# Kernel tuning notes

Hardware: AMD Instinct MI355X
Metric: run time of the kernel (lower is better)

The kernel has to match this reference:

```python
import jax, jax.numpy as jnp
import numpy as np

B, TK, N = 32, 2048, 1024  # batch, encoder steps, 2*hidden_dim


def setup_inputs() -> dict:
    key = jax.random.key(0)
    ks = jax.random.split(key, 12)
    s = 0.02
    return {
        "s_t_hat": jax.random.normal(ks[0], (B, N), jnp.float32),
        "h": jax.random.normal(ks[1], (B, TK, N), jnp.float32),
        "enc_padding_mask": jax.random.uniform(ks[2], (B, TK), jnp.float32),
        "coverage": jax.random.uniform(ks[3], (B, TK), jnp.float32),
        "q_h": jax.random.normal(ks[4], (B, TK, N), jnp.float32),
        "W_h": jax.random.normal(ks[5], (N, N), jnp.float32) * s,
        "W_q": jax.random.normal(ks[6], (N, N), jnp.float32) * s,
        "W_c": jax.random.normal(ks[7], (N,), jnp.float32) * s,   # Linear(1, N) weight, squeezed
        "W_d": jax.random.normal(ks[8], (N, N), jnp.float32) * s,  # decode_proj weight
        "b_d": jnp.zeros((N,), jnp.float32),                       # decode_proj bias
        "v_w": jax.random.normal(ks[9], (N,), jnp.float32) * s,    # v: Linear(N, 1) weight, squeezed
    }


def reference(s_t_hat, h, enc_padding_mask, coverage, q_h, W_h, W_q, W_c, W_d, b_d, v_w):
    # projections (Linear: y = x @ W.T)
    enc_feat = jnp.einsum("btn,mn->btm", h, W_h)            # [B,TK,N]
    q_feat = jnp.einsum("btn,mn->btm", q_h, W_q)            # [B,TK,N]
    dec_feat = s_t_hat @ W_d.T + b_d                         # [B,N]
    cov_feat = coverage[..., None] * W_c                     # [B,TK,N]
    att = jnp.tanh(enc_feat + dec_feat[:, None, :] + q_feat + cov_feat)
    scores = jnp.einsum("btn,n->bt", att, v_w)               # [B,TK]
    attn_ = jax.nn.softmax(scores, axis=1) * enc_padding_mask
    attn = attn_ / jnp.sum(attn_, axis=1, keepdims=True)     # renormalized
    c_t = jnp.einsum("bt,btn->bn", attn, h)                  # context vector
    coverage_out = coverage + attn
    return (c_t, attn, coverage_out)
```

## Files before the change

### kernel.cpp

```cpp
#include <hip/hip_runtime.h>
#include <stdint.h>

#define Bsz 32
#define TKs 2048
#define Nf  1024
#define Msz (Bsz*TKs)
#define KTOT 2048

typedef __bf16 bf16x8 __attribute__((ext_vector_type(8)));
typedef float  f32x4  __attribute__((ext_vector_type(4)));

__device__ __forceinline__ unsigned pack_bf2(float f0, float f1){
  unsigned u0 = __float_as_uint(f0) + 0x8000u;
  unsigned u1 = __float_as_uint(f1) + 0x8000u;
  return __builtin_amdgcn_perm(u1, u0, 0x07060302u);
}

__device__ __forceinline__ float fast_tanh(float x){
  x = fminf(15.f, fmaxf(-15.f, x));
  float e = __expf(2.f * x);
  return (e - 1.f) / (e + 1.f);
}

__device__ __forceinline__ void async16(void* lds, const void* g){
  __builtin_amdgcn_global_load_lds(
      (const __attribute__((address_space(1))) unsigned int*)g,
      (__attribute__((address_space(3))) unsigned int*)lds,
      16, 0, 0);
}

__global__ __launch_bounds__(256) void pack_w_kernel(
    const float* __restrict__ Wh, const float* __restrict__ Wq,
    unsigned short* __restrict__ Wcat)
{
  int idx = (blockIdx.x * 256 + threadIdx.x) * 4;
  int m = idx >> 11;
  int k = idx & 2047;
  const float* src = (k < 1024) ? (Wh + m * 1024 + k) : (Wq + m * 1024 + (k - 1024));
  float4 v = *(const float4*)src;
  uint2 p;
  p.x = pack_bf2(v.x, v.y);
  p.y = pack_bf2(v.z, v.w);
  *(uint2*)(Wcat + idx) = p;
}

__global__ __launch_bounds__(256) void pack_a_kernel(
    const float* __restrict__ h, const float* __restrict__ q,
    unsigned short* __restrict__ Acat)
{
  size_t idx = ((size_t)blockIdx.x * 256 + threadIdx.x) * 8;
  size_t r = idx >> 11;
  int c = (int)(idx & 2047);
  const float* src = (c < 1024) ? (h + r * 1024 + c) : (q + r * 1024 + (c - 1024));
  float4 v0 = ((const float4*)src)[0];
  float4 v1 = ((const float4*)src)[1];
  uint4 p;
  p.x = pack_bf2(v0.x, v0.y); p.y = pack_bf2(v0.z, v0.w);
  p.z = pack_bf2(v1.x, v1.y); p.w = pack_bf2(v1.z, v1.w);
  *(uint4*)(Acat + idx) = p;
}

__global__ __launch_bounds__(256) void dec_kernel(
    const float* __restrict__ s_t, const float* __restrict__ Wd,
    const float* __restrict__ bd, float* __restrict__ dec)
{
  __shared__ float sv[1024];
  const int b = blockIdx.y;
  const int mbase = blockIdx.x * 64;
  for (int i = threadIdx.x; i < 1024; i += 256) sv[i] = s_t[b * 1024 + i];
  __syncthreads();
  const int wave = threadIdx.x >> 6, lane = threadIdx.x & 63;
  #pragma unroll 4
  for (int i = 0; i < 16; ++i){
    int m = mbase + wave * 16 + i;
    const float4* wr = (const float4*)(Wd + (size_t)m * 1024 + lane * 16);
    const float4* sr = (const float4*)(sv + lane * 16);
    float s = 0.f;
    #pragma unroll
    for (int j = 0; j < 4; ++j){
      float4 w = wr[j], x = sr[j];
      s += w.x * x.x + w.y * x.y + w.z * x.z + w.w * x.w;
    }
    #pragma unroll
    for (int d = 1; d < 64; d <<= 1) s += __shfl_xor(s, d);
    if (lane == 0) dec[b * 1024 + m] = s + bd[m];
  }
}

__global__ __launch_bounds__(256) void gemm_fused_fast(
    const unsigned short* __restrict__ Acat,
    const unsigned short* __restrict__ Wcat,
    const float* __restrict__ dec, const float* __restrict__ cov,
    const float* __restrict__ Wc, const float* __restrict__ vw,
    float* __restrict__ scoresP)
{
  __shared__ __align__(16) unsigned short As[128 * 32];
  __shared__ __align__(16) unsigned short Bs[128 * 32];
  __shared__ float ssum[2][128];

  const int tid  = threadIdx.x;
  const int wave = tid >> 6, lane = tid & 63;
  const int wm = wave & 1, wn = wave >> 1;
  const int quad = lane >> 4, low = lane & 15;

  const int p = blockIdx.x;
  const int ntile = (p >> 3) & 7;
  const int mtile = (p & 7) + ((p >> 6) << 3);

  f32x4 acc[4][4];
  #pragma unroll
  for (int i = 0; i < 4; ++i)
    #pragma unroll
    for (int j = 0; j < 4; ++j) acc[i][j] = (f32x4){0.f, 0.f, 0.f, 0.f};

  const int s0 = wave * 128 + lane;
  const int s1 = s0 + 64;
  const unsigned short* pA0 = Acat + (size_t)(mtile * 128 + (s0 >> 2)) * 2048 + (s0 & 3) * 8;
  const unsigned short* pA1 = Acat + (size_t)(mtile * 128 + (s1 >> 2)) * 2048 + (s1 & 3) * 8;
  const unsigned short* pB0 = Wcat + (size_t)(ntile * 128 + (s0 >> 2)) * 2048 + (s0 & 3) * 8;
  const unsigned short* pB1 = Wcat + (size_t)(ntile * 128 + (s1 >> 2)) * 2048 + (s1 & 3) * 8;
  unsigned short* ldsA0 = &As[wave * 512];
  unsigned short* ldsA1 = &As[wave * 512 + 256];
  ldsA1 = &As[wave * 1024 + 512];
  ldsA0 = &As[wave * 1024];
  unsigned short* ldsB0 = &Bs[wave * 1024];
  unsigned short* ldsB1 = &Bs[wave * 1024 + 512];

  const bf16x8* a_rd[4];
  const bf16x8* b_rd[4];
  #pragma unroll
  for (int i = 0; i < 4; ++i){
    a_rd[i] = (const bf16x8*)&As[(wm * 64 + i * 16 + low) * 32 + quad * 8];
    b_rd[i] = (const bf16x8*)&Bs[(wn * 64 + i * 16 + low) * 32 + quad * 8];
  }

  for (int kt = 0; kt < KTOT / 32; ++kt){
    async16(ldsA0, pA0);
    async16(ldsA1, pA1);
    async16(ldsB0, pB0);
    async16(ldsB1, pB1);
    pA0 += 32; pA1 += 32; pB0 += 32; pB1 += 32;
    __syncthreads();
    bf16x8 af[4], bg[4];
    #pragma unroll
    for (int i = 0; i < 4; ++i){ af[i] = *a_rd[i]; bg[i] = *b_rd[i]; }
    #pragma unroll
    for (int mi = 0; mi < 4; ++mi)
      #pragma unroll
      for (int ni = 0; ni < 4; ++ni)
        acc[mi][ni] = __builtin_amdgcn_mfma_f32_16x16x32_bf16(af[mi], bg[ni], acc[mi][ni], 0, 0, 0);
    __syncthreads();
  }

  const int brow = (mtile * 128) >> 11;
  const float* decb = dec + brow * 1024;
  const int colbase = ntile * 128 + wn * 64 + low;
  float dv[4], wc4[4], vw4[4];
  #pragma unroll
  for (int ni = 0; ni < 4; ++ni){
    int col = colbase + ni * 16;
    dv[ni]  = decb[col];
    wc4[ni] = Wc[col];
    vw4[ni] = vw[col];
  }
  const size_t growbase = (size_t)mtile * 128;
  const int rowloc0 = wm * 64 + quad * 4;
  #pragma unroll
  for (int mi = 0; mi < 4; ++mi){
    #pragma unroll
    for (int r = 0; r < 4; ++r){
      int rl = rowloc0 + mi * 16 + r;
      float cv = cov[growbase + rl];
      float s = 0.f;
      #pragma unroll
      for (int ni = 0; ni < 4; ++ni){
        float x = acc[mi][ni][r] + dv[ni] + cv * wc4[ni];
        s += vw4[ni] * fast_tanh(x);
      }
      #pragma unroll
      for (int d = 1; d < 16; d <<= 1) s += __shfl_xor(s, d);
      if (low == 0) ssum[wn][rl] = s;
    }
  }
  __syncthreads();
  if (tid < 128)
    scoresP[(size_t)ntile * Msz + growbase + tid] = ssum[0][tid] + ssum[1][tid];
}

#define AST 40

__global__ __launch_bounds__(256) void gemm_fused_fb(
    const float* __restrict__ h, const float* __restrict__ q,
    const unsigned short* __restrict__ Wcat,
    const float* __restrict__ dec, const float* __restrict__ cov,
    const float* __restrict__ Wc, const float* __restrict__ vw,
    float* __restrict__ scoresP)
{
  __shared__ unsigned short As[128 * AST];
  __shared__ unsigned short Bs[128 * AST];
  __shared__ float ssum[2][128];

  const int tid  = threadIdx.x;
  const int wave = tid >> 6, lane = tid & 63;
  const int wm = wave & 1, wn = wave >> 1;
  const int quad = lane >> 4, low = lane & 15;
  const int ntile = blockIdx.x;
  const int mtile = blockIdx.y;

  f32x4 acc[4][4];
  #pragma unroll
  for (int i = 0; i < 4; ++i)
    #pragma unroll
    for (int j = 0; j < 4; ++j) acc[i][j] = (f32x4){0.f, 0.f, 0.f, 0.f};

  const int sr = tid >> 1;
  const int sh = (tid & 1) * 16;
  const size_t a_goff = ((size_t)(mtile * 128 + sr)) * 1024 + sh;
  const size_t b_goff = ((size_t)(ntile * 128 + sr)) * 2048 + sh;
  unsigned short* a_st = &As[sr * AST + sh];
  unsigned short* b_st = &Bs[sr * AST + sh];

  const bf16x8* a_rd[4];
  const bf16x8* b_rd[4];
  #pragma unroll
  for (int i = 0; i < 4; ++i){
    a_rd[i] = (const bf16x8*)&As[(wm * 64 + i * 16 + low) * AST + quad * 8];
    b_rd[i] = (const bf16x8*)&Bs[(wn * 64 + i * 16 + low) * AST + quad * 8];
  }

  for (int kt = 0; kt < KTOT / 32; ++kt){
    const int k0 = kt * 32;
    {
      const float* src = (k0 < 1024) ? (h + a_goff + k0) : (q + a_goff + (k0 - 1024));
      float4 v0 = ((const float4*)src)[0];
      float4 v1 = ((const float4*)src)[1];
      float4 v2 = ((const float4*)src)[2];
      float4 v3 = ((const float4*)src)[3];
      uint4 p0, p1;
      p0.x = pack_bf2(v0.x, v0.y); p0.y = pack_bf2(v0.z, v0.w);
      p0.z = pack_bf2(v1.x, v1.y); p0.w = pack_bf2(v1.z, v1.w);
      p1.x = pack_bf2(v2.x, v2.y); p1.y = pack_bf2(v2.z, v2.w);
      p1.z = pack_bf2(v3.x, v3.y); p1.w = pack_bf2(v3.z, v3.w);
      ((uint4*)a_st)[0] = p0;
      ((uint4*)a_st)[1] = p1;
    }
    {
      const uint4* src = (const uint4*)(Wcat + b_goff + k0);
      uint4 w0 = src[0];
      uint4 w1 = src[1];
      ((uint4*)b_st)[0] = w0;
      ((uint4*)b_st)[1] = w1;
    }
    __syncthreads();
    bf16x8 af[4], bg[4];
    #pragma unroll
    for (int i = 0; i < 4; ++i){ af[i] = *a_rd[i]; bg[i] = *b_rd[i]; }
    #pragma unroll
    for (int mi = 0; mi < 4; ++mi)
      #pragma unroll
      for (int ni = 0; ni < 4; ++ni)
        acc[mi][ni] = __builtin_amdgcn_mfma_f32_16x16x32_bf16(af[mi], bg[ni], acc[mi][ni], 0, 0, 0);
    __syncthreads();
  }

  const int brow = (mtile * 128) >> 11;
  const float* decb = dec + brow * 1024;
  const int colbase = ntile * 128 + wn * 64 + low;
  float dv[4], wc4[4], vw4[4];
  #pragma unroll
  for (int ni = 0; ni < 4; ++ni){
    int col = colbase + ni * 16;
    dv[ni]  = decb[col];
    wc4[ni] = Wc[col];
    vw4[ni] = vw[col];
  }
  const size_t growbase = (size_t)mtile * 128;
  const int rowloc0 = wm * 64 + quad * 4;
  #pragma unroll
  for (int mi = 0; mi < 4; ++mi){
    #pragma unroll
    for (int r = 0; r < 4; ++r){
      int rl = rowloc0 + mi * 16 + r;
      float cv = cov[growbase + rl];
      float s = 0.f;
      #pragma unroll
      for (int ni = 0; ni < 4; ++ni){
        float x = acc[mi][ni][r] + dv[ni] + cv * wc4[ni];
        s += vw4[ni] * fast_tanh(x);
      }
      #pragma unroll
      for (int d = 1; d < 16; d <<= 1) s += __shfl_xor(s, d);
      if (low == 0) ssum[wn][rl] = s;
    }
  }
  __syncthreads();
  if (tid < 128)
    scoresP[(size_t)ntile * Msz + growbase + tid] = ssum[0][tid] + ssum[1][tid];
}

__global__ __launch_bounds__(256) void softmax_kernel(
    const float* __restrict__ scoresP, const float* __restrict__ mask,
    const float* __restrict__ cov, float* __restrict__ attn_o,
    float* __restrict__ cov_o)
{
  const int b = blockIdx.x;
  const int tid = threadIdx.x;
  const int wave = tid >> 6, lane = tid & 63;
  __shared__ float redm[4], reds[4];
  float sc[8];
  float mx = -3.4e38f;
  #pragma unroll
  for (int j = 0; j < 8; ++j){
    int t = tid + j * 256;
    float s = 0.f;
    #pragma unroll
    for (int p = 0; p < 8; ++p) s += scoresP[(size_t)p * Msz + b * TKs + t];
    sc[j] = s;
    mx = fmaxf(mx, s);
  }
  #pragma unroll
  for (int d = 1; d < 64; d <<= 1) mx = fmaxf(mx, __shfl_xor(mx, d));
  if (lane == 0) redm[wave] = mx;
  __syncthreads();
  mx = fmaxf(fmaxf(redm[0], redm[1]), fmaxf(redm[2], redm[3]));
  float e[8]; float sum = 0.f;
  #pragma unroll
  for (int j = 0; j < 8; ++j){
    int t = tid + j * 256;
    float v = __expf(sc[j] - mx) * mask[b * TKs + t];
    e[j] = v; sum += v;
  }
  #pragma unroll
  for (int d = 1; d < 64; d <<= 1) sum += __shfl_xor(sum, d);
  if (lane == 0) reds[wave] = sum;
  __syncthreads();
  sum = reds[0] + reds[1] + reds[2] + reds[3];
  float inv = 1.f / sum;
  #pragma unroll
  for (int j = 0; j < 8; ++j){
    int t = tid + j * 256;
    float a = e[j] * inv;
    attn_o[b * TKs + t] = a;
    cov_o[b * TKs + t]  = cov[b * TKs + t] + a;
  }
}

__global__ __launch_bounds__(256) void ct_partial(
    const float* __restrict__ h, const float* __restrict__ attn,
    float* __restrict__ P)
{
  const int b = blockIdx.y, tc = blockIdx.x;
  const int n4 = threadIdx.x * 4;
  float4 acc = {0.f, 0.f, 0.f, 0.f};
  const float* hb = h + ((size_t)b * TKs + tc * 64) * Nf;
  const float* ab = attn + b * TKs + tc * 64;
  #pragma unroll 4
  for (int tt = 0; tt < 64; ++tt){
    float a = ab[tt];
    float4 hv = *(const float4*)(hb + (size_t)tt * Nf + n4);
    acc.x += a * hv.x; acc.y += a * hv.y; acc.z += a * hv.z; acc.w += a * hv.w;
  }
  *(float4*)(P + ((size_t)(tc * Bsz + b)) * Nf + n4) = acc;
}

__global__ __launch_bounds__(256) void ct_reduce(
    const float* __restrict__ P, float* __restrict__ out)
{
  int bn = (blockIdx.x * 256 + threadIdx.x) * 4;
  float4 s = {0.f, 0.f, 0.f, 0.f};
  for (int j = 0; j < 32; ++j){
    float4 v = *(const float4*)(P + (size_t)j * (Bsz * Nf) + bn);
    s.x += v.x; s.y += v.y; s.z += v.z; s.w += v.w;
  }
  *(float4*)(out + bn) = s;
}

extern "C" void kernel_launch(void* const* d_in, const int* in_sizes, int n_in,
                              void* d_out, int out_size, void* d_ws, size_t ws_size,
                              hipStream_t stream) {
  const float* s_t  = (const float*)d_in[0];
  const float* h    = (const float*)d_in[1];
  const float* mask = (const float*)d_in[2];
  const float* cov  = (const float*)d_in[3];
  const float* qh   = (const float*)d_in[4];
  const float* Wh   = (const float*)d_in[5];
  const float* Wq   = (const float*)d_in[6];
  const float* Wc   = (const float*)d_in[7];
  const float* Wd   = (const float*)d_in[8];
  const float* bd   = (const float*)d_in[9];
  const float* vw   = (const float*)d_in[10];

  float* out    = (float*)d_out;
  float* c_t    = out;
  float* attn_o = out + Bsz * Nf;
  float* cov_o  = attn_o + Bsz * TKs;

  char* ws = (char*)d_ws;
  unsigned short* Wcat = (unsigned short*)ws;
  float* dec     = (float*)(ws + (4u << 20));
  float* scoresP = (float*)(ws + (4u << 20) + (128u << 10));
  float* ctP     = (float*)(ws + (6u << 20) + (128u << 10));
  unsigned short* Acat = (unsigned short*)(ws + (16ull << 20));

  const size_t need_fast = (16ull << 20) + (size_t)Msz * KTOT * 2;
  const bool fast = (ws_size >= need_fast);

  hipLaunchKernelGGL(pack_w_kernel, dim3(2048), dim3(256), 0, stream, Wh, Wq, Wcat);
  hipLaunchKernelGGL(dec_kernel,    dim3(16, 32), dim3(256), 0, stream, s_t, Wd, bd, dec);
  if (fast){
    hipLaunchKernelGGL(pack_a_kernel, dim3((unsigned)((size_t)Msz * KTOT / 8 / 256)),
                       dim3(256), 0, stream, h, qh, Acat);
    hipLaunchKernelGGL(gemm_fused_fast, dim3(4096), dim3(256), 0, stream,
                       Acat, Wcat, dec, cov, Wc, vw, scoresP);
  } else {
    hipLaunchKernelGGL(gemm_fused_fb, dim3(8, 512), dim3(256), 0, stream,
                       h, qh, Wcat, dec, cov, Wc, vw, scoresP);
  }
  hipLaunchKernelGGL(softmax_kernel, dim3(32), dim3(256), 0, stream,
                     scoresP, mask, cov, attn_o, cov_o);
  hipLaunchKernelGGL(ct_partial, dim3(32, 32), dim3(256), 0, stream, h, attn_o, ctP);
  hipLaunchKernelGGL(ct_reduce,  dim3(32), dim3(256), 0, stream, ctP, c_t);
}
```

Baseline: 992.0 us.

## Switch GEMM to 32x32 MFMA with swizzled LDS, read bf16 h for context

The fused score GEMM moves from 16x16x32 to 32x32x16 bf16 MFMA tiles, and the LDS layout gets an XOR swizzle to reduce bank conflicts. Coverage is staged in shared memory, and tanh uses a reciprocal intrinsic with no clamp. The context-vector partial kernel now reads the bf16 packed copy of h (Acat) instead of fp32 h, roughly halving its traffic. In exchange c_t is computed from bf16-rounded h, which lowers its precision, and the unclamped tanh could give inf/NaN for large inputs in edge cases.

```diff
diff --git a/kernel.cpp b/kernel.cpp
--- a/kernel.cpp
+++ b/kernel.cpp
@@ -9,6 +9,7 @@
 
 typedef __bf16 bf16x8 __attribute__((ext_vector_type(8)));
 typedef float  f32x4  __attribute__((ext_vector_type(4)));
+typedef float  f32x16 __attribute__((ext_vector_type(16)));
 
 __device__ __forceinline__ unsigned pack_bf2(float f0, float f1){
   unsigned u0 = __float_as_uint(f0) + 0x8000u;
@@ -17,9 +18,8 @@
 }
 
 __device__ __forceinline__ float fast_tanh(float x){
-  x = fminf(15.f, fmaxf(-15.f, x));
   float e = __expf(2.f * x);
-  return (e - 1.f) / (e + 1.f);
+  return 1.f - 2.f * __builtin_amdgcn_rcpf(e + 1.f);
 }
 
 __device__ __forceinline__ void async16(void* lds, const void* g){
@@ -97,42 +97,61 @@
   __shared__ __align__(16) unsigned short As[128 * 32];
   __shared__ __align__(16) unsigned short Bs[128 * 32];
   __shared__ float ssum[2][128];
+  __shared__ float covS[128];
 
   const int tid  = threadIdx.x;
   const int wave = tid >> 6, lane = tid & 63;
   const int wm = wave & 1, wn = wave >> 1;
-  const int quad = lane >> 4, low = lane & 15;
+  const int l31 = lane & 31, half = lane >> 5;
 
   const int p = blockIdx.x;
   const int ntile = (p >> 3) & 7;
   const int mtile = (p & 7) + ((p >> 6) << 3);
-
-  f32x4 acc[4][4];
-  #pragma unroll
-  for (int i = 0; i < 4; ++i)
-    #pragma unroll
-    for (int j = 0; j < 4; ++j) acc[i][j] = (f32x4){0.f, 0.f, 0.f, 0.f};
+  const size_t growbase = (size_t)mtile * 128;
+
+  if (tid < 128) covS[tid] = cov[growbase + tid];
+
+  f32x16 acc[2][2];
+  #pragma unroll
+  for (int i = 0; i < 2; ++i)
+    #pragma unroll
+    for (int j = 0; j < 2; ++j)
+      #pragma unroll
+      for (int r = 0; r < 16; ++r) acc[i][j][r] = 0.f;
 
   const int s0 = wave * 128 + lane;
   const int s1 = s0 + 64;
-  const unsigned short* pA0 = Acat + (size_t)(mtile * 128 + (s0 >> 2)) * 2048 + (s0 & 3) * 8;
-  const unsigned short* pA1 = Acat + (size_t)(mtile * 128 + (s1 >> 2)) * 2048 + (s1 & 3) * 8;
-  const unsigned short* pB0 = Wcat + (size_t)(ntile * 128 + (s0 >> 2)) * 2048 + (s0 & 3) * 8;
-  const unsigned short* pB1 = Wcat + (size_t)(ntile * 128 + (s1 >> 2)) * 2048 + (s1 & 3) * 8;
-  unsigned short* ldsA0 = &As[wave * 512];
-  unsigned short* ldsA1 = &As[wave * 512 + 256];
-  ldsA1 = &As[wave * 1024 + 512];
-  ldsA0 = &As[wave * 1024];
+  const int r0 = s0 >> 2, g0 = (s0 & 3) ^ ((r0 >> 1) & 3);
+  const int r1 = s1 >> 2, g1 = (s1 & 3) ^ ((r1 >> 1) & 3);
+  const unsigned short* pA0 = Acat + (size_t)(mtile * 128 + r0) * 2048 + g0 * 8;
+  const unsigned short* pA1 = Acat + (size_t)(mtile * 128 + r1) * 2048 + g1 * 8;
+  const unsigned short* pB0 = Wcat + (size_t)(ntile * 128 + r0) * 2048 + g0 * 8;
+  const unsigned short* pB1 = Wcat + (size_t)(ntile * 128 + r1) * 2048 + g1 * 8;
+  unsigned short* ldsA0 = &As[wave * 1024];
+  unsigned short* ldsA1 = &As[wave * 1024 + 512];
   unsigned short* ldsB0 = &Bs[wave * 1024];
   unsigned short* ldsB1 = &Bs[wave * 1024 + 512];
 
-  const bf16x8* a_rd[4];
-  const bf16x8* b_rd[4];
-  #pragma unroll
-  for (int i = 0; i < 4; ++i){
-    a_rd[i] = (const bf16x8*)&As[(wm * 64 + i * 16 + low) * 32 + quad * 8];
-    b_rd[i] = (const bf16x8*)&Bs[(wn * 64 + i * 16 + low) * 32 + quad * 8];
-  }
+  const bf16x8* a_rd[2][2];
+  const bf16x8* b_rd[2][2];
+  #pragma unroll
+  for (int mi = 0; mi < 2; ++mi)
+    #pragma unroll
+    for (int ks = 0; ks < 2; ++ks){
+      int row = wm * 64 + mi * 32 + l31;
+      int g = ks * 2 + half;
+      int pos = g ^ ((row >> 1) & 3);
+      a_rd[mi][ks] = (const bf16x8*)&As[row * 32 + pos * 8];
+    }
+  #pragma unroll
+  for (int ni = 0; ni < 2; ++ni)
+    #pragma unroll
+    for (int ks = 0; ks < 2; ++ks){
+      int row = wn * 64 + ni * 32 + l31;
+      int g = ks * 2 + half;
+      int pos = g ^ ((row >> 1) & 3);
+      b_rd[ni][ks] = (const bf16x8*)&Bs[row * 32 + pos * 8];
+    }
 
   for (int kt = 0; kt < KTOT / 32; ++kt){
     async16(ldsA0, pA0);
@@ -141,45 +160,47 @@
     async16(ldsB1, pB1);
     pA0 += 32; pA1 += 32; pB0 += 32; pB1 += 32;
     __syncthreads();
-    bf16x8 af[4], bg[4];
-    #pragma unroll
-    for (int i = 0; i < 4; ++i){ af[i] = *a_rd[i]; bg[i] = *b_rd[i]; }
-    #pragma unroll
-    for (int mi = 0; mi < 4; ++mi)
-      #pragma unroll
-      for (int ni = 0; ni < 4; ++ni)
-        acc[mi][ni] = __builtin_amdgcn_mfma_f32_16x16x32_bf16(af[mi], bg[ni], acc[mi][ni], 0, 0, 0);
+    bf16x8 af[2][2], bg[2][2];
+    #pragma unroll
+    for (int i = 0; i < 2; ++i)
+      #pragma unroll
+      for (int ks = 0; ks < 2; ++ks){ af[i][ks] = *a_rd[i][ks]; bg[i][ks] = *b_rd[i][ks]; }
+    #pragma unroll
+    for (int ks = 0; ks < 2; ++ks)
+      #pragma unroll
+      for (int mi = 0; mi < 2; ++mi)
+        #pragma unroll
+        for (int ni = 0; ni < 2; ++ni)
+          acc[mi][ni] = __builtin_amdgcn_mfma_f32_32x32x16_bf16(
+              af[mi][ks], bg[ni][ks], acc[mi][ni], 0, 0, 0);
     __syncthreads();
   }
 
   const int brow = (mtile * 128) >> 11;
   const float* decb = dec + brow * 1024;
-  const int colbase = ntile * 128 + wn * 64 + low;
-  float dv[4], wc4[4], vw4[4];
-  #pragma unroll
-  for (int ni = 0; ni < 4; ++ni){
-    int col = colbase + ni * 16;
+  float dv[2], wc2[2], vw2[2];
+  #pragma unroll
+  for (int ni = 0; ni < 2; ++ni){
+    int col = ntile * 128 + wn * 64 + ni * 32 + l31;
     dv[ni]  = decb[col];
-    wc4[ni] = Wc[col];
-    vw4[ni] = vw[col];
-  }
-  const size_t growbase = (size_t)mtile * 128;
-  const int rowloc0 = wm * 64 + quad * 4;
-  #pragma unroll
-  for (int mi = 0; mi < 4; ++mi){
-    #pragma unroll
-    for (int r = 0; r < 4; ++r){
-      int rl = rowloc0 + mi * 16 + r;
-      float cv = cov[growbase + rl];
+    wc2[ni] = Wc[col];
+    vw2[ni] = vw[col];
+  }
+  #pragma unroll
+  for (int mi = 0; mi < 2; ++mi){
+    #pragma unroll
+    for (int r = 0; r < 16; ++r){
+      int rl = wm * 64 + mi * 32 + (r & 3) + 8 * (r >> 2) + 4 * half;
+      float cv = covS[rl];
       float s = 0.f;
       #pragma unroll
-      for (int ni = 0; ni < 4; ++ni){
-        float x = acc[mi][ni][r] + dv[ni] + cv * wc4[ni];
-        s += vw4[ni] * fast_tanh(x);
+      for (int ni = 0; ni < 2; ++ni){
+        float x = acc[mi][ni][r] + dv[ni] + cv * wc2[ni];
+        s += vw2[ni] * fast_tanh(x);
       }
       #pragma unroll
-      for (int d = 1; d < 16; d <<= 1) s += __shfl_xor(s, d);
-      if (low == 0) ssum[wn][rl] = s;
+      for (int d = 1; d < 32; d <<= 1) s += __shfl_xor(s, d);
+      if (l31 == 0) ssum[wn][rl] = s;
     }
   }
   __syncthreads();
@@ -345,6 +366,27 @@
   }
 }
 
+__global__ __launch_bounds__(256) void ct_partial_bf(
+    const unsigned short* __restrict__ Acat, const float* __restrict__ attn,
+    float* __restrict__ P)
+{
+  const int b = blockIdx.y, tc = blockIdx.x;
+  const int c4 = threadIdx.x * 4;
+  float4 acc = {0.f, 0.f, 0.f, 0.f};
+  const size_t rbase = (size_t)b * TKs + tc * 64;
+  const float* ab = attn + b * TKs + tc * 64;
+  #pragma unroll 4
+  for (int tt = 0; tt < 64; ++tt){
+    float a = ab[tt];
+    uint2 v = *(const uint2*)(Acat + (rbase + tt) * 2048 + c4);
+    acc.x += a * __uint_as_float(v.x << 16);
+    acc.y += a * __uint_as_float(v.x & 0xffff0000u);
+    acc.z += a * __uint_as_float(v.y << 16);
+    acc.w += a * __uint_as_float(v.y & 0xffff0000u);
+  }
+  *(float4*)(P + ((size_t)(tc * Bsz + b)) * Nf + c4) = acc;
+}
+
 __global__ __launch_bounds__(256) void ct_partial(
     const float* __restrict__ h, const float* __restrict__ attn,
     float* __restrict__ P)
@@ -418,6 +460,10 @@
   }
   hipLaunchKernelGGL(softmax_kernel, dim3(32), dim3(256), 0, stream,
                      scoresP, mask, cov, attn_o, cov_o);
-  hipLaunchKernelGGL(ct_partial, dim3(32, 32), dim3(256), 0, stream, h, attn_o, ctP);
+  if (fast){
+    hipLaunchKernelGGL(ct_partial_bf, dim3(32, 32), dim3(256), 0, stream, Acat, attn_o, ctP);
+  } else {
+    hipLaunchKernelGGL(ct_partial, dim3(32, 32), dim3(256), 0, stream, h, attn_o, ctP);
+  }
   hipLaunchKernelGGL(ct_reduce,  dim3(32), dim3(256), 0, stream, ctP, c_t);
 }
```

Result: faster. 961.6 us (-3.1%).
